# Kernel optimization log

Measured on AMD Instinct MI355X. Metric: run time of the kernel, lower is better.

## Reference

```python
import jax, jax.numpy as jnp
import numpy as np
from jax import lax

N = 512      # input_dim (encoder feats)
B = 128      # num_feats (bottleneck)
H = 512      # num_hidden
K = 3        # kernel_size
X = 8        # num_layers per stack
R = 3        # num_stacks
L = X * R    # 24 conv blocks
NSRC = 2
BATCH = 8
T = 3200
EPS = 1e-8


def _gln(x, g, b):
    # GroupNorm(num_groups=1): normalize over (C, T) per sample; x: [B, C, T]
    mean = jnp.mean(x, axis=(1, 2), keepdims=True)
    var = jnp.mean(jnp.square(x - mean), axis=(1, 2), keepdims=True)
    return g[:, None] * (x - mean) * lax.rsqrt(var + EPS) + b[:, None]


def _prelu(x, a):
    return jnp.where(x >= 0, x, a * x)


def _pw(x, W, b):
    # pointwise (1x1) conv: x [B, Cin, T], W [Cout, Cin], b [Cout]
    return jnp.einsum('bct,oc->bot', x, W) + b[:, None]


def _dwconv(x, W, b, dil):
    # depthwise dilated conv, 'same' length (pad = dil for K=3): W [H, K]
    out = lax.conv_general_dilated(
        x, W[:, None, :], window_strides=(1,), padding=[(dil, dil)],
        rhs_dilation=(dil,), dimension_numbers=('NCH', 'OIH', 'NCH'),
        feature_group_count=H)
    return out + b[:, None]


def setup_inputs() -> dict:
    key = jax.random.key(0)
    ks = jax.random.split(key, 12)
    s = 0.02
    inp = {
        'x': jax.random.normal(ks[0], (BATCH, N, T), jnp.float32),
        'in_g': jnp.ones((N,), jnp.float32),
        'in_b': jnp.zeros((N,), jnp.float32),
        'Wc': jax.random.normal(ks[1], (B, N), jnp.float32) * s,
        'bc': jnp.zeros((B,), jnp.float32),
        'W1': jax.random.normal(ks[2], (L, H, B), jnp.float32) * s,
        'b1': jnp.zeros((L, H), jnp.float32),
        'a1': jnp.full((L,), 0.25, jnp.float32),
        'g1': jnp.ones((L, H), jnp.float32),
        'be1': jnp.zeros((L, H), jnp.float32),
        'Wd': jax.random.normal(ks[3], (L, H, K), jnp.float32) * s,
        'bd': jnp.zeros((L, H), jnp.float32),
        'a2': jnp.full((L,), 0.25, jnp.float32),
        'g2': jnp.ones((L, H), jnp.float32),
        'be2': jnp.zeros((L, H), jnp.float32),
        'Wres': jax.random.normal(ks[4], (L, B, H), jnp.float32) * s,
        'bres': jnp.zeros((L, B), jnp.float32),
        'Wskip': jax.random.normal(ks[5], (L, B, H), jnp.float32) * s,
        'bskip': jnp.zeros((L, B), jnp.float32),
        'a_out': jnp.asarray(0.25, jnp.float32),
        'Wo': jax.random.normal(ks[6], (NSRC * N, B), jnp.float32) * s,
        'bo': jnp.zeros((NSRC * N,), jnp.float32),
    }
    return inp


def reference(x, in_g, in_b, Wc, bc, W1, b1, a1, g1, be1, Wd, bd, a2, g2, be2,
              Wres, bres, Wskip, bskip, a_out, Wo, bo):
    feats = _gln(x, in_g, in_b)            # input GroupNorm(1, N)
    feats = _pw(feats, Wc, bc)             # [B, Bfeat, T]
    output = jnp.zeros_like(feats)
    for i in range(L):
        dil = 2 ** (i % X)
        h = _pw(feats, W1[i], b1[i])                 # 1x1: B -> H
        h = _gln(_prelu(h, a1[i]), g1[i], be1[i])
        h = _dwconv(h, Wd[i], bd[i], dil)            # depthwise dilated
        h = _gln(_prelu(h, a2[i]), g2[i], be2[i])
        output = output + _pw(h, Wskip[i], bskip[i])
        if i < L - 1:                                # last block: no residual
            feats = feats + _pw(h, Wres[i], bres[i])
    out = _prelu(output, a_out)
    out = _pw(out, Wo, bo)                 # [B, NSRC*N, T]
    out = jax.nn.sigmoid(out)
    return out.reshape(x.shape[0], NSRC, N, -1)
```

## Files before the change

### kernel.cpp

```cpp
#include <hip/hip_runtime.h>
#include <cstdint>
#include <cstddef>

#define BATCHN 8
#define TLEN   3200
#define NCH    512
#define BCH    128
#define HCH    512
#define LBLK   24
#define CNTF   (512.0f * 3200.0f)
#define EPSV   1e-8f
#define NSLOT  32

typedef float  floatx4 __attribute__((ext_vector_type(4)));
typedef short  short8  __attribute__((ext_vector_type(8)));
typedef short  short4v __attribute__((ext_vector_type(4)));

enum { EP_FIRST = 1, EP_LAST = 2 };

__device__ inline unsigned short f2bf(float f) {
    unsigned int u = __float_as_uint(f);
    u = (u + 0x7fffu + ((u >> 16) & 1u)) >> 16;
    return (unsigned short)u;
}
__device__ inline float bf2f(short s) {
    return __uint_as_float(((unsigned int)(unsigned short)s) << 16);
}

__device__ inline void gload_lds16(const unsigned short* g, unsigned short* l) {
    __builtin_amdgcn_global_load_lds(
        (const __attribute__((address_space(1))) unsigned int*)(g),
        (__attribute__((address_space(3))) unsigned int*)(l),
        16, 0, 0);
}

__device__ inline void block_reduce_atomic2(float s, float ss, float* out) {
#pragma unroll
    for (int off = 32; off; off >>= 1) {
        s  += __shfl_down(s, off, 64);
        ss += __shfl_down(ss, off, 64);
    }
    __shared__ float pr[16];
    const int wave = threadIdx.x >> 6;
    const int lane = threadIdx.x & 63;
    if (lane == 0) { pr[wave * 2] = s; pr[wave * 2 + 1] = ss; }
    __syncthreads();
    if (threadIdx.x == 0) {
        const int nw = blockDim.x >> 6;
        float a = 0.f, b = 0.f;
        for (int i = 0; i < nw; i++) { a += pr[i * 2]; b += pr[i * 2 + 1]; }
        atomicAdd(out, a);
        atomicAdd(out + 1, b);
    }
}

__device__ inline void load_stats32(const float* __restrict__ st,
                                    float& mu, float& rstd) {
    float s = 0.f, ss = 0.f;
#pragma unroll
    for (int i = 0; i < NSLOT; i++) { s += st[2 * i]; ss += st[2 * i + 1]; }
    mu = s * (1.f / CNTF);
    const float var = ss * (1.f / CNTF) - mu * mu;
    rstd = rsqrtf(var + EPSV);
}

template <int KDIM, int EP>
__global__ __launch_bounds__(256, 4) void mm_k(
    const unsigned short* __restrict__ X,
    const unsigned short* __restrict__ W,
    const float* __restrict__ bias, const float* __restrict__ uv,
    float* __restrict__ O_f32, unsigned short* __restrict__ O_bf,
    const float* __restrict__ outAcc_ro,
    const float* __restrict__ statsIn,
    const float* __restrict__ alphaPtr, int Cout)
{
    const int b    = blockIdx.z;
    const int t0   = blockIdx.x * 128;
    const int m0   = blockIdx.y * 128;
    const int lane = threadIdx.x & 63;
    const int wid  = threadIdx.x >> 6;
    const int wt   = wid & 1;
    const int wm   = wid >> 1;
    const int l15  = lane & 15;
    const int quad = lane >> 4;

    const unsigned short* Xb =
        X + ((size_t)b * TLEN + t0 + wt * 64 + l15) * KDIM + quad * 8;
    const unsigned short* Wb =
        W + (size_t)(m0 + wm * 64 + l15) * KDIM + quad * 8;

    floatx4 acc[4][4];
#pragma unroll
    for (int i = 0; i < 4; i++)
#pragma unroll
        for (int j = 0; j < 4; j++)
#pragma unroll
            for (int r = 0; r < 4; r++) acc[i][j][r] = 0.f;

#pragma unroll 2
    for (int kc = 0; kc < KDIM / 32; ++kc) {
        const int ko = kc * 32;
        short8 a[4], w[4];
#pragma unroll
        for (int i = 0; i < 4; i++)
            a[i] = *reinterpret_cast<const short8*>(Xb + (size_t)i * 16 * KDIM + ko);
#pragma unroll
        for (int j = 0; j < 4; j++)
            w[j] = *reinterpret_cast<const short8*>(Wb + (size_t)j * 16 * KDIM + ko);
#pragma unroll
        for (int i = 0; i < 4; i++)
#pragma unroll
            for (int j = 0; j < 4; j++)
                acc[i][j] = __builtin_amdgcn_mfma_f32_16x16x32_bf16(
                    w[j], a[i], acc[i][j], 0, 0, 0);
    }

    float mu = 0.f, rstd = 1.f, alpha = 0.f;
    load_stats32(statsIn + b * (2 * NSLOT), mu, rstd);
    if (EP == EP_LAST) alpha = alphaPtr[0];

#pragma unroll
    for (int j = 0; j < 4; j++) {
        const int cb = m0 + wm * 64 + j * 16 + quad * 4;
        const float4 b4 = *reinterpret_cast<const float4*>(bias + cb);
        const float4 u4 = *reinterpret_cast<const float4*>(uv + cb);
        const float4 v4 = *reinterpret_cast<const float4*>(
            uv + cb + (EP == EP_LAST ? 2 * BCH : Cout));
        float rb[4] = { b4.x + u4.x - mu * rstd * v4.x,
                        b4.y + u4.y - mu * rstd * v4.y,
                        b4.z + u4.z - mu * rstd * v4.z,
                        b4.w + u4.w - mu * rstd * v4.w };
#pragma unroll
        for (int i = 0; i < 4; i++) {
            const int t = t0 + wt * 64 + i * 16 + l15;
            const size_t idx = ((size_t)b * TLEN + t) * Cout + cb;
            if (EP == EP_FIRST) {
                float4 o;
                short4v s;
#pragma unroll
                for (int r = 0; r < 4; r++) {
                    const float val = rstd * acc[i][j][r] + rb[r];
                    (&o.x)[r] = val;
                    s[r] = (short)f2bf(val);
                }
                *reinterpret_cast<float4*>(O_f32 + idx) = o;
                *reinterpret_cast<short4v*>(O_bf + idx) = s;
            } else {
                const float4 oa = *reinterpret_cast<const float4*>(outAcc_ro + idx);
                short4v s;
#pragma unroll
                for (int r = 0; r < 4; r++) {
                    const float val = rstd * acc[i][j][r] + rb[r];
                    const float f = (&oa.x)[r] + val;
                    const float pv = f >= 0.f ? f : alpha * f;
                    s[r] = (short)f2bf(pv);
                }
                *reinterpret_cast<short4v*>(O_bf + idx) = s;
            }
        }
    }
}

__global__ __launch_bounds__(256, 4) void mm_h_lds_k(
    const unsigned short* __restrict__ X,
    const unsigned short* __restrict__ W,
    const float* __restrict__ bias,
    float* __restrict__ statsOut,
    const float* __restrict__ alphaPtr,
    unsigned short* __restrict__ O_bf)
{
    __shared__ unsigned short As[128 * 128];
    const int b    = blockIdx.z;
    const int t0   = blockIdx.x * 128;
    const int m0   = blockIdx.y * 128;
    const int lane = threadIdx.x & 63;
    const int wid  = threadIdx.x >> 6;
    const int wt   = wid & 1;
    const int wm   = wid >> 1;
    const int l15  = lane & 15;
    const int quad = lane >> 4;

#pragma unroll
    for (int q = 0; q < 8; q++) {
        const int r = wid * 32 + q * 4 + quad;
        const unsigned short* src =
            X + ((size_t)b * TLEN + t0 + r) * BCH + ((l15 ^ (r & 15)) * 8);
        gload_lds16(src, As + (wid * 32 + q * 4) * BCH);
    }
    __syncthreads();

    const unsigned short* Wb =
        W + (size_t)(m0 + wm * 64 + l15) * BCH + quad * 8;

    floatx4 acc[4][4];
#pragma unroll
    for (int i = 0; i < 4; i++)
#pragma unroll
        for (int j = 0; j < 4; j++)
#pragma unroll
            for (int r = 0; r < 4; r++) acc[i][j][r] = 0.f;

#pragma unroll
    for (int kc = 0; kc < 4; ++kc) {
        short8 a[4], w[4];
#pragma unroll
        for (int j = 0; j < 4; j++)
            w[j] = *reinterpret_cast<const short8*>(
                Wb + (size_t)j * 16 * BCH + kc * 32);
#pragma unroll
        for (int i = 0; i < 4; i++) {
            const int R  = wt * 64 + i * 16 + l15;
            const int sl = (kc * 4 + quad) ^ l15;
            a[i] = *reinterpret_cast<const short8*>(As + R * BCH + sl * 8);
        }
#pragma unroll
        for (int i = 0; i < 4; i++)
#pragma unroll
            for (int j = 0; j < 4; j++)
                acc[i][j] = __builtin_amdgcn_mfma_f32_16x16x32_bf16(
                    w[j], a[i], acc[i][j], 0, 0, 0);
    }

    const float alpha = alphaPtr[0];
    float ssum = 0.f, ssq = 0.f;
#pragma unroll
    for (int j = 0; j < 4; j++) {
        const int cb = m0 + wm * 64 + j * 16 + quad * 4;
        const float4 b4 = *reinterpret_cast<const float4*>(bias + cb);
#pragma unroll
        for (int i = 0; i < 4; i++) {
            const int t = t0 + wt * 64 + i * 16 + l15;
            short4v s;
#pragma unroll
            for (int r = 0; r < 4; r++) {
                float val = acc[i][j][r] + (&b4.x)[r];
                val = val >= 0.f ? val : alpha * val;
                ssum += val; ssq += val * val;
                s[r] = (short)f2bf(val);
            }
            *reinterpret_cast<short4v*>(
                O_bf + ((size_t)b * TLEN + t) * HCH + cb) = s;
        }
    }
    block_reduce_atomic2(ssum, ssq,
        statsOut + b * (2 * NSLOT) +
        ((blockIdx.x + blockIdx.y * 25) & (NSLOT - 1)) * 2);
}

__global__ __launch_bounds__(512, 4) void mm_dual_h_k(
    const unsigned short* __restrict__ X,
    const unsigned short* __restrict__ Wsr,
    const float* __restrict__ bskip, const float* __restrict__ bres,
    const float* __restrict__ uv,
    float* __restrict__ feats,
    float* __restrict__ outAcc,
    const float* __restrict__ statsIn,
    const unsigned short* __restrict__ W1,
    const float* __restrict__ b1,
    const float* __restrict__ a1p,
    float* __restrict__ statsOut,
    unsigned short* __restrict__ h_out)
{
    __shared__ unsigned short As[2][64 * 128];
    const int b    = blockIdx.z;
    const int t0   = blockIdx.x * 64;
    const int lane = threadIdx.x & 63;
    const int wv   = threadIdx.x >> 6;
    const int l15  = lane & 15;
    const int quad = lane >> 4;

    const unsigned short* Wb =
        Wsr + (size_t)(wv * 32 + l15) * HCH + quad * 8;

    floatx4 acc[4][2];
#pragma unroll
    for (int i = 0; i < 4; i++)
#pragma unroll
        for (int j = 0; j < 2; j++)
#pragma unroll
            for (int r = 0; r < 4; r++) acc[i][j][r] = 0.f;

    const int srow = wv * 8;
#define STAGE_CHUNK(KC, BUF)                                                  \
    {                                                                         \
        _Pragma("unroll")                                                     \
        for (int q = 0; q < 2; q++) {                                         \
            const int r = srow + q * 4 + quad;                                \
            const unsigned short* src =                                       \
                X + ((size_t)b * TLEN + t0 + r) * HCH + (KC) * 128 +          \
                ((l15 ^ (r & 15)) * 8);                                       \
            gload_lds16(src, As[BUF] + (srow + q * 4) * 128);                 \
        }                                                                     \
    }

    STAGE_CHUNK(0, 0);
    __syncthreads();

#pragma unroll
    for (int kc = 0; kc < 4; ++kc) {
        if (kc < 3) STAGE_CHUNK(kc + 1, (kc + 1) & 1);
        const unsigned short* Ab = As[kc & 1];
#pragma unroll
        for (int ks = 0; ks < 4; ++ks) {
            short8 a[4], w[2];
#pragma unroll
            for (int j = 0; j < 2; j++)
                w[j] = *reinterpret_cast<const short8*>(
                    Wb + (size_t)j * 16 * HCH + kc * 128 + ks * 32);
#pragma unroll
            for (int i = 0; i < 4; i++) {
                const int R  = i * 16 + l15;
                const int sl = (ks * 4 + quad) ^ l15;
                a[i] = *reinterpret_cast<const short8*>(Ab + R * 128 + sl * 8);
            }
#pragma unroll
            for (int i = 0; i < 4; i++)
#pragma unroll
                for (int j = 0; j < 2; j++)
                    acc[i][j] = __builtin_amdgcn_mfma_f32_16x16x32_bf16(
                        w[j], a[i], acc[i][j], 0, 0, 0);
        }
        __syncthreads();
    }
#undef STAGE_CHUNK

    float mu, rstd;
    load_stats32(statsIn + b * (2 * NSLOT), mu, rstd);

    const bool sk = (wv < 4);
#pragma unroll
    for (int j = 0; j < 2; j++) {
        const int c  = wv * 32 + j * 16 + quad * 4;
        const int cc = sk ? c : c - 128;
        const float4 b4 = sk
            ? *reinterpret_cast<const float4*>(bskip + cc)
            : *reinterpret_cast<const float4*>(bres + cc);
        const float4 u4 = *reinterpret_cast<const float4*>(uv + c);
        const float4 v4 = *reinterpret_cast<const float4*>(uv + c + 256);
        float rb[4] = { b4.x + u4.x - mu * rstd * v4.x,
                        b4.y + u4.y - mu * rstd * v4.y,
                        b4.z + u4.z - mu * rstd * v4.z,
                        b4.w + u4.w - mu * rstd * v4.w };
#pragma unroll
        for (int i = 0; i < 4; i++) {
            const int t = t0 + i * 16 + l15;
            const size_t idx = ((size_t)b * TLEN + t) * BCH + cc;
            if (sk) {
                float4 oa = *reinterpret_cast<const float4*>(outAcc + idx);
#pragma unroll
                for (int r = 0; r < 4; r++)
                    (&oa.x)[r] += rstd * acc[i][j][r] + rb[r];
                *reinterpret_cast<float4*>(outAcc + idx) = oa;
            } else {
                float4 f = *reinterpret_cast<const float4*>(feats + idx);
                short4v s;
#pragma unroll
                for (int r = 0; r < 4; r++) {
                    (&f.x)[r] += rstd * acc[i][j][r] + rb[r];
                    s[r] = (short)f2bf((&f.x)[r]);
                }
                *reinterpret_cast<float4*>(feats + idx) = f;
                const int row = i * 16 + l15;
                const int sl  = (cc >> 3) ^ l15;
                *reinterpret_cast<short4v*>(
                    As[0] + row * 128 + sl * 8 + (cc & 7)) = s;
            }
        }
    }
    __syncthreads();

    const float alpha1 = a1p[0];
    float ssum = 0.f, ssq = 0.f;
    const int mb = wv * 64;
    const unsigned short* W1p =
        W1 + (size_t)(mb + l15) * BCH + quad * 8;

    floatx4 acc2[4][4];
#pragma unroll
    for (int i = 0; i < 4; i++)
#pragma unroll
        for (int j = 0; j < 4; j++)
#pragma unroll
            for (int r = 0; r < 4; r++) acc2[i][j][r] = 0.f;

#pragma unroll
    for (int kc = 0; kc < 4; ++kc) {
        short8 a[4], w[4];
#pragma unroll
        for (int j = 0; j < 4; j++)
            w[j] = *reinterpret_cast<const short8*>(
                W1p + (size_t)j * 16 * BCH + kc * 32);
#pragma unroll
        for (int i = 0; i < 4; i++) {
            const int R  = i * 16 + l15;
            const int sl = (kc * 4 + quad) ^ l15;
            a[i] = *reinterpret_cast<const short8*>(As[0] + R * 128 + sl * 8);
        }
#pragma unroll
        for (int i = 0; i < 4; i++)
#pragma unroll
            for (int j = 0; j < 4; j++)
                acc2[i][j] = __builtin_amdgcn_mfma_f32_16x16x32_bf16(
                    w[j], a[i], acc2[i][j], 0, 0, 0);
    }

#pragma unroll
    for (int j = 0; j < 4; j++) {
        const int cb = mb + j * 16 + quad * 4;
        const float4 b4 = *reinterpret_cast<const float4*>(b1 + cb);
#pragma unroll
        for (int i = 0; i < 4; i++) {
            const int t = t0 + i * 16 + l15;
            short4v s;
#pragma unroll
            for (int r = 0; r < 4; r++) {
                float val = acc2[i][j][r] + (&b4.x)[r];
                val = val >= 0.f ? val : alpha1 * val;
                ssum += val; ssq += val * val;
                s[r] = (short)f2bf(val);
            }
            *reinterpret_cast<short4v*>(
                h_out + ((size_t)b * TLEN + t) * HCH + cb) = s;
        }
    }
    block_reduce_atomic2(ssum, ssq,
        statsOut + b * (2 * NSLOT) + (blockIdx.x & (NSLOT - 1)) * 2);
}

__global__ __launch_bounds__(256, 4) void mm_final_k(
    const unsigned short* __restrict__ Xbf, const unsigned short* __restrict__ Wb,
    const float* __restrict__ bo, float* __restrict__ out)
{
    const int b    = blockIdx.z;
    const int t0   = blockIdx.x * 128;
    const int m0   = blockIdx.y * 128;
    const int lane = threadIdx.x & 63;
    const int wid  = threadIdx.x >> 6;
    const int wc   = wid & 1;
    const int wr   = wid >> 1;
    const int l15  = lane & 15;
    const int quad = lane >> 4;

    const unsigned short* Wp =
        Wb + (size_t)(m0 + wr * 64 + l15) * BCH + quad * 8;
    const unsigned short* Xp =
        Xbf + ((size_t)b * TLEN + t0 + wc * 64 + l15) * BCH + quad * 8;

    floatx4 acc[4][4];
#pragma unroll
    for (int i = 0; i < 4; i++)
#pragma unroll
        for (int j = 0; j < 4; j++)
#pragma unroll
            for (int r = 0; r < 4; r++) acc[i][j][r] = 0.f;

#pragma unroll 2
    for (int kc = 0; kc < BCH / 32; ++kc) {
        const int ko = kc * 32;
        short8 a[4], x[4];
#pragma unroll
        for (int i = 0; i < 4; i++)
            a[i] = *reinterpret_cast<const short8*>(Wp + (size_t)i * 16 * BCH + ko);
#pragma unroll
        for (int j = 0; j < 4; j++)
            x[j] = *reinterpret_cast<const short8*>(Xp + (size_t)j * 16 * BCH + ko);
#pragma unroll
        for (int i = 0; i < 4; i++)
#pragma unroll
            for (int j = 0; j < 4; j++)
                acc[i][j] = __builtin_amdgcn_mfma_f32_16x16x32_bf16(
                    a[i], x[j], acc[i][j], 0, 0, 0);
    }

#pragma unroll
    for (int i = 0; i < 4; i++) {
        const int mb = m0 + wr * 64 + i * 16 + quad * 4;
#pragma unroll
        for (int r = 0; r < 4; r++) {
            const int m = mb + r;
            const float bz = bo[m];
#pragma unroll
            for (int j = 0; j < 4; j++) {
                const int t = t0 + wc * 64 + j * 16 + l15;
                const float val = acc[i][j][r] + bz;
                const float e = __expf(-val);
                out[((size_t)b * (2 * NCH) + m) * TLEN + t] =
                    __builtin_amdgcn_rcpf(1.f + e);
            }
        }
    }
}

__global__ __launch_bounds__(256) void prep_w_k(
    const float* __restrict__ W, const float* __restrict__ g,
    const float* __restrict__ be, unsigned short* __restrict__ Wout,
    float* __restrict__ uv, int Mrows, int K, int nmat, int Mout, int rowOff)
{
    const int r    = blockIdx.x * 4 + (threadIdx.x >> 6);
    const int lane = threadIdx.x & 63;
    if (r >= Mrows * nmat) return;
    const int mat = r / Mrows;
    const int m   = r - mat * Mrows;
    const float* Wrow = W + (size_t)r * K;
    const float* gv = g  ? g  + (size_t)mat * K : nullptr;
    const float* bv = be ? be + (size_t)mat * K : nullptr;
    unsigned short* orow = Wout + ((size_t)mat * Mout + rowOff + m) * K;
    float u = 0.f, v = 0.f;
    for (int k = lane * 4; k < K; k += 256) {
        float4 w4 = *reinterpret_cast<const float4*>(Wrow + k);
        float4 o4 = w4;
        if (gv) {
            const float4 g4 = *reinterpret_cast<const float4*>(gv + k);
            const float4 b4 = *reinterpret_cast<const float4*>(bv + k);
            o4.x = w4.x * g4.x; o4.y = w4.y * g4.y;
            o4.z = w4.z * g4.z; o4.w = w4.w * g4.w;
            u += w4.x * b4.x + w4.y * b4.y + w4.z * b4.z + w4.w * b4.w;
            v += w4.x * g4.x + w4.y * g4.y + w4.z * g4.z + w4.w * g4.w;
        }
        short4v s;
        s[0] = (short)f2bf(o4.x); s[1] = (short)f2bf(o4.y);
        s[2] = (short)f2bf(o4.z); s[3] = (short)f2bf(o4.w);
        *reinterpret_cast<short4v*>(orow + k) = s;
    }
    if (gv && uv) {
#pragma unroll
        for (int off = 32; off; off >>= 1) {
            u += __shfl_down(u, off, 64);
            v += __shfl_down(v, off, 64);
        }
        if (lane == 0) {
            uv[(size_t)mat * 2 * Mout + rowOff + m]        = u;
            uv[(size_t)mat * 2 * Mout + Mout + rowOff + m] = v;
        }
    }
}

__global__ __launch_bounds__(256) void tr_x_k(
    const float* __restrict__ x, unsigned short* __restrict__ xt,
    float* __restrict__ statsOut)
{
    __shared__ unsigned short tile[32][33];
    const int b  = blockIdx.z;
    const int t0 = blockIdx.x * 32;
    const int c0 = blockIdx.y * 32;
    const int tx = threadIdx.x & 31;
    const int ty = threadIdx.x >> 5;

    float s = 0.f, ss = 0.f;
#pragma unroll
    for (int r = 0; r < 4; r++) {
        const int cl = ty + r * 8;
        const float v = x[((size_t)b * NCH + c0 + cl) * TLEN + t0 + tx];
        s += v; ss += v * v;
        tile[tx][cl] = f2bf(v);
    }
    __syncthreads();
#pragma unroll
    for (int r = 0; r < 4; r++) {
        const int tl = ty + r * 8;
        xt[((size_t)b * TLEN + t0 + tl) * NCH + c0 + tx] = tile[tl][tx];
    }
    block_reduce_atomic2(s, ss,
        statsOut + b * (2 * NSLOT) +
        ((blockIdx.x + blockIdx.y * 25) & (NSLOT - 1)) * 2);
}

__global__ __launch_bounds__(256) void dwconv_k(
    const unsigned short* __restrict__ h, unsigned short* __restrict__ hd,
    const float* __restrict__ Wd, const float* __restrict__ bd,
    const float* __restrict__ g1, const float* __restrict__ be1,
    const float* __restrict__ statsIn, float* __restrict__ statsOut,
    const float* __restrict__ a2p, int dil)
{
    const int b  = blockIdx.y;
    const int tb = blockIdx.x * 16 + (threadIdx.x >> 6) * 4;
    const int c0 = (threadIdx.x & 63) * 8;

    float mu, rstd;
    load_stats32(statsIn + b * (2 * NSLOT), mu, rstd);
    const float alpha = a2p[0];

    float g[8], be[8], bz[8], wall[24];
#pragma unroll
    for (int q = 0; q < 6; q++) {
        const float4 w4 = *reinterpret_cast<const float4*>(Wd + (size_t)c0 * 3 + q * 4);
        wall[q * 4 + 0] = w4.x; wall[q * 4 + 1] = w4.y;
        wall[q * 4 + 2] = w4.z; wall[q * 4 + 3] = w4.w;
    }
    {
        const float4 ga = *reinterpret_cast<const float4*>(g1 + c0);
        const float4 gb = *reinterpret_cast<const float4*>(g1 + c0 + 4);
        const float4 ba = *reinterpret_cast<const float4*>(be1 + c0);
        const float4 bb = *reinterpret_cast<const float4*>(be1 + c0 + 4);
        const float4 da = *reinterpret_cast<const float4*>(bd + c0);
        const float4 db = *reinterpret_cast<const float4*>(bd + c0 + 4);
        const float gg[8] = { ga.x, ga.y, ga.z, ga.w, gb.x, gb.y, gb.z, gb.w };
        const float bbv[8] = { ba.x, ba.y, ba.z, ba.w, bb.x, bb.y, bb.z, bb.w };
        const float dd[8] = { da.x, da.y, da.z, da.w, db.x, db.y, db.z, db.w };
#pragma unroll
        for (int jj = 0; jj < 8; jj++) {
            g[jj]  = gg[jj] * rstd;
            be[jj] = bbv[jj] - mu * rstd * gg[jj];
            bz[jj] = dd[jj];
        }
    }

    float psum = 0.f, psq = 0.f;
#pragma unroll
    for (int it = 0; it < 4; ++it) {
        const int t = tb + it;
        const size_t rowb = ((size_t)b * TLEN + t) * HCH + c0;
        const bool hasP = (t - dil) >= 0;
        const bool hasN = (t + dil) < TLEN;
        const short8 cur = *reinterpret_cast<const short8*>(h + rowb);
        short8 prv = {}, nxt = {};
        if (hasP) prv = *reinterpret_cast<const short8*>(h + rowb - (size_t)dil * HCH);
        if (hasN) nxt = *reinterpret_cast<const short8*>(h + rowb + (size_t)dil * HCH);

        short8 o;
#pragma unroll
        for (int jj = 0; jj < 8; jj++) {
            float acc = bz[jj] + wall[jj * 3 + 1] * (g[jj] * bf2f(cur[jj]) + be[jj]);
            if (hasP) acc += wall[jj * 3 + 0] * (g[jj] * bf2f(prv[jj]) + be[jj]);
            if (hasN) acc += wall[jj * 3 + 2] * (g[jj] * bf2f(nxt[jj]) + be[jj]);
            const float v = acc >= 0.f ? acc : alpha * acc;
            o[jj] = (short)f2bf(v);
            psum += v; psq += v * v;
        }
        *reinterpret_cast<short8*>(hd + rowb) = o;
    }
    block_reduce_atomic2(psum, psq,
        statsOut + b * (2 * NSLOT) + (blockIdx.x & (NSLOT - 1)) * 2);
}

extern "C" void kernel_launch(void* const* d_in, const int* in_sizes, int n_in,
                              void* d_out, int out_size, void* d_ws, size_t ws_size,
                              hipStream_t stream)
{
    (void)in_sizes; (void)n_in; (void)out_size; (void)ws_size;

    const float* x    = (const float*)d_in[0];
    const float* in_g = (const float*)d_in[1];
    const float* in_b = (const float*)d_in[2];
    const float* Wc   = (const float*)d_in[3];
    const float* bc   = (const float*)d_in[4];
    const float* W1   = (const float*)d_in[5];
    const float* b1   = (const float*)d_in[6];
    const float* a1   = (const float*)d_in[7];
    const float* g1   = (const float*)d_in[8];
    const float* be1  = (const float*)d_in[9];
    const float* Wd   = (const float*)d_in[10];
    const float* bd   = (const float*)d_in[11];
    const float* a2   = (const float*)d_in[12];
    const float* g2   = (const float*)d_in[13];
    const float* be2  = (const float*)d_in[14];
    const float* Wres = (const float*)d_in[15];
    const float* bres = (const float*)d_in[16];
    const float* Wskip= (const float*)d_in[17];
    const float* bskip= (const float*)d_in[18];
    const float* aout = (const float*)d_in[19];
    const float* Wo   = (const float*)d_in[20];
    const float* bo   = (const float*)d_in[21];
    float* out = (float*)d_out;

    uint8_t* p = (uint8_t*)d_ws;
    unsigned short* x_t      = (unsigned short*)p; p += (size_t)BATCHN*TLEN*NCH*2;
    float*          feats    = (float*)p;          p += (size_t)BATCHN*TLEN*BCH*4;
    unsigned short* feats_bf = (unsigned short*)p; p += (size_t)BATCHN*TLEN*BCH*2;
    float*          outAcc   = (float*)p;          p += (size_t)BATCHN*TLEN*BCH*4;
    unsigned short* h        = (unsigned short*)p; p += (size_t)BATCHN*TLEN*HCH*2;
    unsigned short* hd       = (unsigned short*)p; p += (size_t)BATCHN*TLEN*HCH*2;
    unsigned short* WcG      = (unsigned short*)p; p += (size_t)BCH*NCH*2;
    unsigned short* W1b      = (unsigned short*)p; p += (size_t)LBLK*HCH*BCH*2;
    unsigned short* Wsr      = (unsigned short*)p; p += (size_t)LBLK*256*HCH*2;
    unsigned short* Wob      = (unsigned short*)p; p += (size_t)(2*NCH)*BCH*2;
    float*          uv_c     = (float*)p;          p += (size_t)2*BCH*4;
    float*          uv_sr    = (float*)p;          p += (size_t)LBLK*2*256*4;
    float*          stats    = (float*)p;

    const size_t SLOTF = (size_t)BATCHN * 2 * NSLOT;

    hipMemsetAsync(stats, 0, (size_t)49 * SLOTF * sizeof(float), stream);
    hipMemsetAsync(outAcc, 0, (size_t)BATCHN*TLEN*BCH*sizeof(float), stream);

    tr_x_k<<<dim3(100, 16, BATCHN), 256, 0, stream>>>(x, x_t, stats);
    prep_w_k<<<32,   256, 0, stream>>>(Wc,   in_g,    in_b,    WcG, uv_c, BCH,   NCH, 1,      BCH, 0);
    prep_w_k<<<3072, 256, 0, stream>>>(W1,   nullptr, nullptr, W1b, nullptr, HCH, BCH, LBLK,  HCH, 0);
    prep_w_k<<<768,  256, 0, stream>>>(Wskip,g2,      be2,     Wsr, uv_sr, BCH,  HCH, LBLK,   256, 0);
    prep_w_k<<<736,  256, 0, stream>>>(Wres, g2,      be2,     Wsr, uv_sr, BCH,  HCH, LBLK-1, 256, 128);
    prep_w_k<<<256,  256, 0, stream>>>(Wo,   nullptr, nullptr, Wob, nullptr, 2*NCH, BCH, 1,   2*NCH, 0);

    mm_k<NCH, EP_FIRST><<<dim3(25, 1, BATCHN), 256, 0, stream>>>(
        x_t, WcG, bc, uv_c, feats, feats_bf, nullptr, stats, nullptr, BCH);

    mm_h_lds_k<<<dim3(25, 4, BATCHN), 256, 0, stream>>>(
        feats_bf, W1b, b1, stats + SLOTF, a1, h);

    for (int i = 0; i < LBLK; i++) {
        float* st_h  = stats + (size_t)(1 + 2 * i) * SLOTF;
        float* st_hd = stats + (size_t)(2 + 2 * i) * SLOTF;
        const int dil = 1 << (i & 7);

        dwconv_k<<<dim3(TLEN / 16, BATCHN), 256, 0, stream>>>(
            h, hd, Wd + (size_t)i * HCH * 3, bd + (size_t)i * HCH,
            g1 + (size_t)i * HCH, be1 + (size_t)i * HCH,
            st_h, st_hd, a2 + i, dil);

        if (i < LBLK - 1) {
            mm_dual_h_k<<<dim3(50, 1, BATCHN), 512, 0, stream>>>(
                hd, Wsr + (size_t)i * 256 * HCH,
                bskip + (size_t)i * BCH, bres + (size_t)i * BCH,
                uv_sr + (size_t)i * 2 * 256,
                feats, outAcc, st_hd,
                W1b + (size_t)(i + 1) * HCH * BCH,
                b1 + (size_t)(i + 1) * HCH, a1 + (i + 1),
                stats + (size_t)(1 + 2 * (i + 1)) * SLOTF, h);
        } else {
            mm_k<HCH, EP_LAST><<<dim3(25, 1, BATCHN), 256, 0, stream>>>(
                hd, Wsr + (size_t)i * 256 * HCH,
                bskip + (size_t)i * BCH, uv_sr + (size_t)i * 2 * 256,
                nullptr, feats_bf, outAcc, st_hd, aout, BCH);
        }
    }

    mm_final_k<<<dim3(25, 8, BATCHN), 256, 0, stream>>>(
        feats_bf, Wob, bo, out);
}
```

Baseline: 1.755 ms.

## Fuse depthwise conv into dual matmul kernel with grid-wide barrier

Each layer's depthwise dilated conv (GroupNorm, conv, PReLU) now runs inside the skip/residual matmul kernel. The conv result goes straight into shared memory as the matmul A-tile, so the intermediate hd tensor is never written to or read back from global memory and one launch per layer disappears. A global atomic-counter spin barrier waits until every block has contributed to the GroupNorm statistics before the matmul epilogue uses them. This only works if all 400 blocks are co-resident, and the spin barrier adds synchronisation cost.

```diff
diff --git a/kernel.cpp b/kernel.cpp
--- a/kernel.cpp
+++ b/kernel.cpp
@@ -11,6 +11,7 @@
 #define CNTF   (512.0f * 3200.0f)
 #define EPSV   1e-8f
 #define NSLOT  32
+#define NBLK   400
 
 typedef float  floatx4 __attribute__((ext_vector_type(4)));
 typedef short  short8  __attribute__((ext_vector_type(8)));
@@ -25,13 +26,6 @@
 }
 __device__ inline float bf2f(short s) {
     return __uint_as_float(((unsigned int)(unsigned short)s) << 16);
-}
-
-__device__ inline void gload_lds16(const unsigned short* g, unsigned short* l) {
-    __builtin_amdgcn_global_load_lds(
-        (const __attribute__((address_space(1))) unsigned int*)(g),
-        (__attribute__((address_space(3))) unsigned int*)(l),
-        16, 0, 0);
 }
 
 __device__ inline void block_reduce_atomic2(float s, float ss, float* out) {
@@ -59,6 +53,18 @@
     float s = 0.f, ss = 0.f;
 #pragma unroll
     for (int i = 0; i < NSLOT; i++) { s += st[2 * i]; ss += st[2 * i + 1]; }
+    mu = s * (1.f / CNTF);
+    const float var = ss * (1.f / CNTF) - mu * mu;
+    rstd = rsqrtf(var + EPSV);
+}
+
+__device__ inline void load_stats32_coh(const float* st, float& mu, float& rstd) {
+    float s = 0.f, ss = 0.f;
+#pragma unroll
+    for (int i = 0; i < NSLOT; i++) {
+        s  += __hip_atomic_load(st + 2 * i,     __ATOMIC_RELAXED, __HIP_MEMORY_SCOPE_AGENT);
+        ss += __hip_atomic_load(st + 2 * i + 1, __ATOMIC_RELAXED, __HIP_MEMORY_SCOPE_AGENT);
+    }
     mu = s * (1.f / CNTF);
     const float var = ss * (1.f / CNTF) - mu * mu;
     rstd = rsqrtf(var + EPSV);
@@ -161,6 +167,13 @@
     }
 }
 
+__device__ inline void gload_lds16(const unsigned short* g, unsigned short* l) {
+    __builtin_amdgcn_global_load_lds(
+        (const __attribute__((address_space(1))) unsigned int*)(g),
+        (__attribute__((address_space(3))) unsigned int*)(l),
+        16, 0, 0);
+}
+
 __global__ __launch_bounds__(256, 4) void mm_h_lds_k(
     const unsigned short* __restrict__ X,
     const unsigned short* __restrict__ W,
@@ -247,21 +260,21 @@
         ((blockIdx.x + blockIdx.y * 25) & (NSLOT - 1)) * 2);
 }
 
-__global__ __launch_bounds__(512, 4) void mm_dual_h_k(
-    const unsigned short* __restrict__ X,
+__global__ __launch_bounds__(512, 4) void layer_k(
+    unsigned short* __restrict__ h,
+    const float* __restrict__ Wd, const float* __restrict__ bd,
+    const float* __restrict__ g1v, const float* __restrict__ be1v,
+    const float* __restrict__ st_h_in, const float* __restrict__ a2p, int dil,
     const unsigned short* __restrict__ Wsr,
     const float* __restrict__ bskip, const float* __restrict__ bres,
     const float* __restrict__ uv,
-    float* __restrict__ feats,
-    float* __restrict__ outAcc,
-    const float* __restrict__ statsIn,
+    float* __restrict__ st_hd, unsigned int* __restrict__ ctr,
+    float* __restrict__ feats, float* __restrict__ outAcc,
     const unsigned short* __restrict__ W1,
-    const float* __restrict__ b1,
-    const float* __restrict__ a1p,
-    float* __restrict__ statsOut,
-    unsigned short* __restrict__ h_out)
+    const float* __restrict__ b1, const float* __restrict__ a1p,
+    float* __restrict__ st_h_next)
 {
-    __shared__ unsigned short As[2][64 * 128];
+    __shared__ unsigned short As[4 * 64 * 128];
     const int b    = blockIdx.z;
     const int t0   = blockIdx.x * 64;
     const int lane = threadIdx.x & 63;
@@ -269,6 +282,80 @@
     const int l15  = lane & 15;
     const int quad = lane >> 4;
 
+    {
+        float mu1, rstd1;
+        load_stats32(st_h_in + b * (2 * NSLOT), mu1, rstd1);
+        const float alpha = a2p[0];
+        const int c0 = lane * 8;
+        float g[8], be[8], bz[8], wall[24];
+#pragma unroll
+        for (int qq = 0; qq < 6; qq++) {
+            const float4 w4 = *reinterpret_cast<const float4*>(Wd + (size_t)c0 * 3 + qq * 4);
+            wall[qq * 4 + 0] = w4.x; wall[qq * 4 + 1] = w4.y;
+            wall[qq * 4 + 2] = w4.z; wall[qq * 4 + 3] = w4.w;
+        }
+        {
+            const float4 ga = *reinterpret_cast<const float4*>(g1v + c0);
+            const float4 gb = *reinterpret_cast<const float4*>(g1v + c0 + 4);
+            const float4 ba = *reinterpret_cast<const float4*>(be1v + c0);
+            const float4 bb = *reinterpret_cast<const float4*>(be1v + c0 + 4);
+            const float4 da = *reinterpret_cast<const float4*>(bd + c0);
+            const float4 db = *reinterpret_cast<const float4*>(bd + c0 + 4);
+            const float gg[8]  = { ga.x, ga.y, ga.z, ga.w, gb.x, gb.y, gb.z, gb.w };
+            const float bbv[8] = { ba.x, ba.y, ba.z, ba.w, bb.x, bb.y, bb.z, bb.w };
+            const float dd[8]  = { da.x, da.y, da.z, da.w, db.x, db.y, db.z, db.w };
+#pragma unroll
+            for (int jj = 0; jj < 8; jj++) {
+                g[jj]  = gg[jj] * rstd1;
+                be[jj] = bbv[jj] - mu1 * rstd1 * gg[jj];
+                bz[jj] = dd[jj];
+            }
+        }
+        float psum = 0.f, psq = 0.f;
+        const int chunk = c0 >> 7;
+        const int cc    = c0 & 127;
+#pragma unroll
+        for (int q = 0; q < 8; ++q) {
+            const int rl = wv * 8 + q;
+            const int t  = t0 + rl;
+            const size_t rowb = ((size_t)b * TLEN + t) * HCH + c0;
+            const bool hasP = (t - dil) >= 0;
+            const bool hasN = (t + dil) < TLEN;
+            const short8 cur = *reinterpret_cast<const short8*>(h + rowb);
+            short8 prv = {}, nxt = {};
+            if (hasP) prv = *reinterpret_cast<const short8*>(h + rowb - (size_t)dil * HCH);
+            if (hasN) nxt = *reinterpret_cast<const short8*>(h + rowb + (size_t)dil * HCH);
+            short8 o;
+#pragma unroll
+            for (int jj = 0; jj < 8; jj++) {
+                float a0 = bz[jj] + wall[jj * 3 + 1] * (g[jj] * bf2f(cur[jj]) + be[jj]);
+                if (hasP) a0 += wall[jj * 3 + 0] * (g[jj] * bf2f(prv[jj]) + be[jj]);
+                if (hasN) a0 += wall[jj * 3 + 2] * (g[jj] * bf2f(nxt[jj]) + be[jj]);
+                const float v = a0 >= 0.f ? a0 : alpha * a0;
+                o[jj] = (short)f2bf(v);
+                psum += v; psq += v * v;
+            }
+            *reinterpret_cast<short8*>(
+                As + chunk * 8192 + rl * 128 + (((cc >> 3) ^ (rl & 15)) * 8)) = o;
+        }
+        block_reduce_atomic2(psum, psq,
+            st_hd + b * (2 * NSLOT) + (blockIdx.x & (NSLOT - 1)) * 2);
+    }
+
+    __syncthreads();
+    if (threadIdx.x == 0) {
+        __hip_atomic_fetch_add(ctr, 1u, __ATOMIC_ACQ_REL, __HIP_MEMORY_SCOPE_AGENT);
+        unsigned int v;
+        do {
+            __builtin_amdgcn_s_sleep(2);
+            v = __hip_atomic_load(ctr, __ATOMIC_ACQUIRE, __HIP_MEMORY_SCOPE_AGENT);
+        } while (v < (unsigned)NBLK);
+    }
+    __syncthreads();
+
+    float mu, rstd;
+    load_stats32_coh(st_hd + b * (2 * NSLOT), mu, rstd);
+
     const unsigned short* Wb =
         Wsr + (size_t)(wv * 32 + l15) * HCH + quad * 8;
 
@@ -280,26 +367,9 @@
 #pragma unroll
             for (int r = 0; r < 4; r++) acc[i][j][r] = 0.f;
 
-    const int srow = wv * 8;
-#define STAGE_CHUNK(KC, BUF)                                                  \
-    {                                                                         \
-        _Pragma("unroll")                                                     \
-        for (int q = 0; q < 2; q++) {                                         \
-            const int r = srow + q * 4 + quad;                                \
-            const unsigned short* src =                                       \
-                X + ((size_t)b * TLEN + t0 + r) * HCH + (KC) * 128 +          \
-                ((l15 ^ (r & 15)) * 8);                                       \
-            gload_lds16(src, As[BUF] + (srow + q * 4) * 128);                 \
-        }                                                                     \
-    }
-
-    STAGE_CHUNK(0, 0);
-    __syncthreads();
-
 #pragma unroll
     for (int kc = 0; kc < 4; ++kc) {
-        if (kc < 3) STAGE_CHUNK(kc + 1, (kc + 1) & 1);
-        const unsigned short* Ab = As[kc & 1];
+        const unsigned short* Ab = As + kc * 8192;
 #pragma unroll
         for (int ks = 0; ks < 4; ++ks) {
             short8 a[4], w[2];
@@ -320,12 +390,8 @@
                     acc[i][j] = __builtin_amdgcn_mfma_f32_16x16x32_bf16(
                         w[j], a[i], acc[i][j], 0, 0, 0);
         }
-        __syncthreads();
-    }
-#undef STAGE_CHUNK
-
-    float mu, rstd;
-    load_stats32(statsIn + b * (2 * NSLOT), mu, rstd);
+    }
+    __syncthreads();
 
     const bool sk = (wv < 4);
 #pragma unroll
@@ -363,7 +429,7 @@
                 const int row = i * 16 + l15;
                 const int sl  = (cc >> 3) ^ l15;
                 *reinterpret_cast<short4v*>(
-                    As[0] + row * 128 + sl * 8 + (cc & 7)) = s;
+                    As + row * 128 + sl * 8 + (cc & 7)) = s;
             }
         }
     }
@@ -394,7 +460,7 @@
         for (int i = 0; i < 4; i++) {
             const int R  = i * 16 + l15;
             const int sl = (kc * 4 + quad) ^ l15;
-            a[i] = *reinterpret_cast<const short8*>(As[0] + R * 128 + sl * 8);
+            a[i] = *reinterpret_cast<const short8*>(As + R * 128 + sl * 8);
         }
 #pragma unroll
         for (int i = 0; i < 4; i++)
@@ -420,11 +486,11 @@
                 s[r] = (short)f2bf(val);
             }
             *reinterpret_cast<short4v*>(
-                h_out + ((size_t)b * TLEN + t) * HCH + cb) = s;
+                h + ((size_t)b * TLEN + t) * HCH + cb) = s;
         }
     }
     block_reduce_atomic2(ssum, ssq,
-        statsOut + b * (2 * NSLOT) + (blockIdx.x & (NSLOT - 1)) * 2);
+        st_h_next + b * (2 * NSLOT) + (blockIdx.x & (NSLOT - 1)) * 2);
 }
 
 __global__ __launch_bounds__(256, 4) void mm_final_k(
@@ -679,8 +745,11 @@
     float*          stats    = (float*)p;
 
     const size_t SLOTF = (size_t)BATCHN * 2 * NSLOT;
-
-    hipMemsetAsync(stats, 0, (size_t)49 * SLOTF * sizeof(float), stream);
+    unsigned int* ctrs = (unsigned int*)(stats + 49 * SLOTF);
+
+    hipMemsetAsync(stats, 0,
+                   (size_t)49 * SLOTF * sizeof(float) + 32 * sizeof(unsigned int),
+                   stream);
     hipMemsetAsync(outAcc, 0, (size_t)BATCHN*TLEN*BCH*sizeof(float), stream);
 
     tr_x_k<<<dim3(100, 16, BATCHN), 256, 0, stream>>>(x, x_t, stats);
@@ -701,21 +770,25 @@
         float* st_hd = stats + (size_t)(2 + 2 * i) * SLOTF;
         const int dil = 1 << (i & 7);
 
-        dwconv_k<<<dim3(TLEN / 16, BATCHN), 256, 0, stream>>>(
-            h, hd, Wd + (size_t)i * HCH * 3, bd + (size_t)i * HCH,
-            g1 + (size_t)i * HCH, be1 + (size_t)i * HCH,
-            st_h, st_hd, a2 + i, dil);
-
         if (i < LBLK - 1) {
-            mm_dual_h_k<<<dim3(50, 1, BATCHN), 512, 0, stream>>>(
-                hd, Wsr + (size_t)i * 256 * HCH,
+            layer_k<<<dim3(50, 1, BATCHN), 512, 0, stream>>>(
+                h,
+                Wd + (size_t)i * HCH * 3, bd + (size_t)i * HCH,
+                g1 + (size_t)i * HCH, be1 + (size_t)i * HCH,
+                st_h, a2 + i, dil,
+                Wsr + (size_t)i * 256 * HCH,
                 bskip + (size_t)i * BCH, bres + (size_t)i * BCH,
                 uv_sr + (size_t)i * 2 * 256,
-                feats, outAcc, st_hd,
+                st_hd, ctrs + i,
+                feats, outAcc,
                 W1b + (size_t)(i + 1) * HCH * BCH,
                 b1 + (size_t)(i + 1) * HCH, a1 + (i + 1),
-                stats + (size_t)(1 + 2 * (i + 1)) * SLOTF, h);
+                stats + (size_t)(1 + 2 * (i + 1)) * SLOTF);
         } else {
+            dwconv_k<<<dim3(TLEN / 16, BATCHN), 256, 0, stream>>>(
+                h, hd, Wd + (size_t)i * HCH * 3, bd + (size_t)i * HCH,
+                g1 + (size_t)i * HCH, be1 + (size_t)i * HCH,
+                st_h, st_hd, a2 + i, dil);
             mm_k<HCH, EP_LAST><<<dim3(25, 1, BATCHN), 256, 0, stream>>>(
                 hd, Wsr + (size_t)i * 256 * HCH,
                 bskip + (size_t)i * BCH, uv_sr + (size_t)i * 2 * 256,
```

Measured after the change: 3.031 ms. 72.7% more time.
